# Kernel tuning notes

Measured on AMD Instinct MI355X. Metric: run time of the kernel, lower is better.

Reference implementation:

```python
import jax, jax.numpy as jnp
import numpy as np
from jax import lax

D = 256      # d_model
NH = 4       # nhead == len(multi_size)
DH = D // NH # per-head dim = 64
B, H, W = 8, 32, 32
EPS_LN = 1e-5
EPS_ATT = 1e-6


def conv2d(x, w, pad):
    # x: [B,C,H,W], w: [O,I,k,k], SAME padding via pad=k//2
    return lax.conv_general_dilated(
        x, w, window_strides=(1, 1), padding=[(pad, pad), (pad, pad)],
        dimension_numbers=("NCHW", "OIHW", "NCHW"))


def layer_norm(x, g, b):
    m = jnp.mean(x, axis=-1, keepdims=True)
    v = jnp.mean((x - m) ** 2, axis=-1, keepdims=True)
    return (x - m) * lax.rsqrt(v + EPS_LN) * g + b


def setup_inputs() -> dict:
    key = jax.random.key(0)
    ks = jax.random.split(key, 20)
    s = 0.02
    inp = {
        "x": jax.random.normal(ks[0], (B, D, H, W), jnp.float32),
        "source": jax.random.normal(ks[1], (B, D, H, W), jnp.float32),
        # q projection: conv3x3 d_model -> d_model (bias-free)
        "Wq": jax.random.normal(ks[2], (D, D, 3, 3), jnp.float32) * s,
        # MultiConv k projection: kernels 1,3,5,7, each d_model -> dim
        "Wk1": jax.random.normal(ks[3], (DH, D, 1, 1), jnp.float32) * s,
        "Wk3": jax.random.normal(ks[4], (DH, D, 3, 3), jnp.float32) * s,
        "Wk5": jax.random.normal(ks[5], (DH, D, 5, 5), jnp.float32) * s,
        "Wk7": jax.random.normal(ks[6], (DH, D, 7, 7), jnp.float32) * s,
        # MultiConv v projection
        "Wv1": jax.random.normal(ks[7], (DH, D, 1, 1), jnp.float32) * s,
        "Wv3": jax.random.normal(ks[8], (DH, D, 3, 3), jnp.float32) * s,
        "Wv5": jax.random.normal(ks[9], (DH, D, 5, 5), jnp.float32) * s,
        "Wv7": jax.random.normal(ks[10], (DH, D, 7, 7), jnp.float32) * s,
        # merge linear (bias=False), stored [in,out]
        "Wm": jax.random.normal(ks[11], (D, D), jnp.float32) * s,
        "ln1_g": jnp.ones((D,), jnp.float32),
        "ln1_b": jnp.zeros((D,), jnp.float32),
        "ln2_g": jnp.ones((D,), jnp.float32),
        "ln2_b": jnp.zeros((D,), jnp.float32),
        # FF mlp: Linear(2D->2D, no bias), ReLU, Linear(2D->D, no bias); [in,out]
        "W1": jax.random.normal(ks[12], (2 * D, 2 * D), jnp.float32) * s,
        "W2": jax.random.normal(ks[13], (2 * D, D), jnp.float32) * s,
    }
    return inp


def _forward(x, source, Wq, Wk1, Wk3, Wk5, Wk7, Wv1, Wv3, Wv5, Wv7,
             Wm, ln1_g, ln1_b, ln2_g, ln2_b, W1, W2):
    b, c, h, w = x.shape
    h1, w1 = source.shape[2], source.shape[3]
    L = h * w
    S = h1 * w1

    # projections (multi-scale convs -> heads along channel)
    q = conv2d(x, Wq, 1)                                        # [b,D,h,w]
    k = jnp.concatenate([conv2d(source, Wk1, 0), conv2d(source, Wk3, 1),
                         conv2d(source, Wk5, 2), conv2d(source, Wk7, 3)], axis=1)
    v = jnp.concatenate([conv2d(source, Wv1, 0), conv2d(source, Wv3, 1),
                         conv2d(source, Wv5, 2), conv2d(source, Wv7, 3)], axis=1)

    # b c h w -> b (h w) (nhead dim) -> b L nhead dim
    q = q.transpose(0, 2, 3, 1).reshape(b, L, NH, DH)
    k = k.transpose(0, 2, 3, 1).reshape(b, S, NH, DH)
    v = v.transpose(0, 2, 3, 1).reshape(b, S, NH, DH)

    # FullAttention_vis: softmax attention map [b, L, S, nhead]
    temp = DH ** -0.5
    qk = jnp.einsum("blhd,bshd->blsh", q, k)
    attn_vis = jax.nn.softmax(qk * temp, axis=2)

    # LinearAttention (elu+1 kernel feature map)
    Qf = jax.nn.elu(q) + 1.0
    Kf = jax.nn.elu(k) + 1.0
    v_len = jnp.float32(S)
    vals = v / v_len
    KV = jnp.einsum("bshd,bshv->bhdv", Kf, vals)                # [b,NH,DH,DH]
    Z = 1.0 / (jnp.einsum("blhd,bhd->blh", Qf, Kf.sum(axis=1)) + EPS_ATT)
    msg = jnp.einsum("blhd,bhdv,blh->blhv", Qf, KV, Z) * v_len  # [b,L,NH,DH]

    # merge + norm1
    msg = layer_norm(msg.reshape(b, L, D) @ Wm, ln1_g, ln1_b)

    # FF (mlp): cat -> Linear -> ReLU -> Linear -> norm2
    xf = x.transpose(0, 2, 3, 1).reshape(b, L, c)
    ff = jax.nn.relu(jnp.concatenate([xf, msg], axis=2) @ W1) @ W2
    msg = layer_norm(ff, ln2_g, ln2_b)                          # [b,L,D]
    msg = msg.reshape(b, h, w, c).transpose(0, 3, 1, 2)         # b c h w

    out = x + msg
    # b (h0 w0) (h1 w1) c -> b c h0 w0 h1 w1
    vis = attn_vis.reshape(b, h, w, h1, w1, NH).transpose(0, 5, 1, 2, 3, 4)
    return out, vis


def reference(x, source, Wq, Wk1, Wk3, Wk5, Wk7, Wv1, Wv3, Wv5, Wv7,
              Wm, ln1_g, ln1_b, ln2_g, ln2_b, W1, W2):
    return _forward(x, source, Wq, Wk1, Wk3, Wk5, Wk7, Wv1, Wv3, Wv5, Wv7,
                    Wm, ln1_g, ln1_b, ln2_g, ln2_b, W1, W2)
```

## Files before the change

kernel.cpp:

```cpp
#include <hip/hip_runtime.h>

#define DEV __device__ __forceinline__

typedef unsigned short u16;
typedef unsigned int u32;
typedef __bf16 bf16x8 __attribute__((ext_vector_type(8)));
typedef float f32x4 __attribute__((ext_vector_type(4)));

DEV float elu1(float x) { return x > 0.f ? x + 1.f : __expf(x); }

DEV u16 f2bf(float f) {
    union { float f; unsigned u; } v; v.f = f;
    unsigned r = v.u + 0x7fffu + ((v.u >> 16) & 1u);
    return (u16)(r >> 16);
}

__global__ __launch_bounds__(256) void repack_kernel(
    const float* __restrict__ Wq,
    const float* __restrict__ Wk1, const float* __restrict__ Wk3,
    const float* __restrict__ Wk5, const float* __restrict__ Wk7,
    const float* __restrict__ Wv1, const float* __restrict__ Wv3,
    const float* __restrict__ Wv5, const float* __restrict__ Wv7,
    u16* __restrict__ wpack)
{
    int gid = blockIdx.x * 256 + threadIdx.x;
    int frag = gid >> 6, l = gid & 63;
    const float* W; int K, ocbase = 0, rel;
    if (frag < 1152) {
        W = Wq; K = 3; int slot = frag / 288; rel = frag % 288; ocbase = slot * 64;
    } else {
        int f = frag - 1152; int side = f / 2688; f %= 2688;
        if (f < 32)        { W = side ? Wv1 : Wk1; K = 1; rel = f; }
        else if (f < 320)  { W = side ? Wv3 : Wk3; K = 3; rel = f - 32; }
        else if (f < 1120) { W = side ? Wv5 : Wk5; K = 5; rel = f - 320; }
        else               { W = side ? Wv7 : Wk7; K = 7; rel = f - 1120; }
    }
    int og = rel & 3, cc = (rel >> 2) & 7, tap = rel >> 5;
    int dy = tap / K, dx = tap % K;
    int oc = ocbase + og * 16 + (l & 15);
    int c0 = cc * 32 + (l >> 4) * 8;
    u16 pk[8];
#pragma unroll
    for (int j = 0; j < 8; ++j)
        pk[j] = f2bf(W[((size_t)(oc * 256 + c0 + j) * K + dy) * K + dx]);
    *(int4*)&wpack[(size_t)frag * 512 + l * 8] = *(const int4*)pk;
}

__global__ __launch_bounds__(256) void cast_src_kernel(
    const float* __restrict__ x, const float* __restrict__ src,
    u16* __restrict__ xbh, u16* __restrict__ sbh)
{
    __shared__ float lds[32 * 129];
    const int i = blockIdx.x, t = threadIdx.x;
    const int inp = i >> 9, rem = i & 511;
    const int b = rem >> 6, cc = (rem >> 3) & 7, pxb = rem & 7;
    const float* in = (inp ? src : x) + ((size_t)b * 256 + cc * 32) * 1024 + pxb * 128;
    u16* outp = (inp ? sbh : xbh) + (size_t)b * 262144 + (size_t)cc * 32768 + pxb * 128 * 32;
#pragma unroll
    for (int u = 0; u < 4; ++u) {
        int unit = t + u * 256;
        int r = unit >> 5, px4 = unit & 31;
        float4 v = *(const float4*)(in + (size_t)r * 1024 + px4 * 4);
        lds[r * 129 + px4 * 4 + 0] = v.x;
        lds[r * 129 + px4 * 4 + 1] = v.y;
        lds[r * 129 + px4 * 4 + 2] = v.z;
        lds[r * 129 + px4 * 4 + 3] = v.w;
    }
    __syncthreads();
#pragma unroll
    for (int u = 0; u < 2; ++u) {
        int unit = t + u * 256;
        int px = unit >> 2, cg = unit & 3;
        u16 pk[8];
#pragma unroll
        for (int j = 0; j < 8; ++j) pk[j] = f2bf(lds[(cg * 8 + j) * 129 + px]);
        *(int4*)&outp[px * 32 + cg * 8] = *(const int4*)pk;
    }
}

__global__ __launch_bounds__(256) void cast_qk_kernel(
    const float* __restrict__ qb, const float* __restrict__ kb,
    u16* __restrict__ qbt, u16* __restrict__ kbt)
{
    __shared__ float lds[64 * 65];
    const int i = blockIdx.x, t = threadIdx.x;
    const int inp = i >> 9, rem = i & 511;
    const int b = rem >> 6, h = (rem >> 4) & 3, pxb = rem & 15;
    const float* in = (inp ? kb : qb) + ((size_t)b * 256 + h * 64) * 1024 + pxb * 64;
    u16* outp = (inp ? kbt : qbt) + (((size_t)(b * 4 + h)) * 1024 + pxb * 64) * 64;
#pragma unroll
    for (int u = 0; u < 4; ++u) {
        int unit = t + u * 256;
        int r = unit >> 4, px4 = unit & 15;
        float4 v = *(const float4*)(in + (size_t)r * 1024 + px4 * 4);
        lds[r * 65 + px4 * 4 + 0] = v.x;
        lds[r * 65 + px4 * 4 + 1] = v.y;
        lds[r * 65 + px4 * 4 + 2] = v.z;
        lds[r * 65 + px4 * 4 + 3] = v.w;
    }
    __syncthreads();
#pragma unroll
    for (int u = 0; u < 2; ++u) {
        int unit = t + u * 256;
        int px = unit >> 3, cg = unit & 7;
        u16 pk[8];
#pragma unroll
        for (int j = 0; j < 8; ++j) pk[j] = f2bf(lds[(cg * 8 + j) * 65 + px]);
        *(int4*)&outp[px * 64 + cg * 8] = *(const int4*)pk;
    }
}

__global__ __launch_bounds__(256) void repack_ff_kernel(
    const float* __restrict__ W1, const float* __restrict__ W2,
    const float* __restrict__ Wm,
    u16* __restrict__ w1p, u16* __restrict__ w2p, u16* __restrict__ wmp)
{
    int gid = blockIdx.x * 256 + threadIdx.x;
    int f = gid >> 6, l = gid & 63;
    if (f >= 896) return;
    u16 pk[8];
    if (f < 512) {
        int ks = f >> 5, nf = f & 31;
#pragma unroll
        for (int j = 0; j < 8; ++j)
            pk[j] = f2bf(W1[(size_t)(ks * 32 + (l >> 4) * 8 + j) * 512 + nf * 16 + (l & 15)]);
        *(int4*)&w1p[(size_t)f * 512 + l * 8] = *(const int4*)pk;
    } else if (f < 768) {
        int f2 = f - 512;
        int ks = f2 >> 4, nf = f2 & 15;
#pragma unroll
        for (int j = 0; j < 8; ++j)
            pk[j] = f2bf(W2[(size_t)(ks * 32 + (l >> 4) * 8 + j) * 256 + nf * 16 + (l & 15)]);
        *(int4*)&w2p[(size_t)f2 * 512 + l * 8] = *(const int4*)pk;
    } else {
        int f3 = f - 768;
        int ks = f3 >> 4, nf = f3 & 15;
#pragma unroll
        for (int j = 0; j < 8; ++j)
            pk[j] = f2bf(Wm[(size_t)(ks * 32 + (l >> 4) * 8 + j) * 256 + nf * 16 + (l & 15)]);
        *(int4*)&wmp[(size_t)f3 * 512 + l * 8] = *(const int4*)pk;
    }
}

template<int K>
DEV void conv_mfma_body(const u16* __restrict__ srcb,
                        const u16* __restrict__ wsec,
                        float* __restrict__ dst,
                        u16* Bt, int y0, int cch0, int ncc, int t)
{
    constexpr int P = K / 2;
    const int w = t >> 6, l = t & 63;
    const int chi = l >> 4, ln = l & 15;
    const int rowbase = chi * 22 + w * 2 + 3 - P;
    const int colbase = ln + 3 - P;
    f32x4 acc[4][4];
#pragma unroll
    for (int m = 0; m < 4; ++m)
#pragma unroll
        for (int n = 0; n < 4; ++n) acc[m][n] = (f32x4){0.f, 0.f, 0.f, 0.f};

    for (int cc = 0; cc < ncc; ++cc) {
        const int ccg = cch0 + cc;
        __syncthreads();
#pragma unroll
        for (int u = 0; u < 7; ++u) {
            int unit = t + (u << 9);
            if (unit < 2816) {
                int xv = unit & 31, r = unit >> 5;
                int yy = r % 22, ch = r / 22;
                int ygl = y0 - 3 + yy;
                int4 pk;
                if ((unsigned)ygl < 32u)
                    pk = *(const int4*)&srcb[(size_t)ccg * 32768 + (ygl * 32 + xv) * 32 + ch * 8];
                else
                    pk = (int4){0, 0, 0, 0};
                *(int4*)&Bt[((ch * 22 + yy) * 40 + xv + 3) * 8] = pk;
            } else if (unit < 3520) {
                int hu = unit - 2816;
                int hx = hu & 7; int xi = hx < 3 ? hx : hx + 32;
                int r = hu >> 3; int yy = r % 22, ch = r / 22;
                int4 z = {0, 0, 0, 0};
                *(int4*)&Bt[((ch * 22 + yy) * 40 + xi) * 8] = z;
            }
        }
        __syncthreads();
#pragma unroll
        for (int dy = 0; dy < K; ++dy) {
#pragma unroll
            for (int dx = 0; dx < K; ++dx) {
                const int tap = dy * K + dx;
                const u16* wp = wsec + ((size_t)(tap * 8 + ccg) * 4) * 512 + l * 8;
                bf16x8 a0 = *(const bf16x8*)(wp);
                bf16x8 a1 = *(const bf16x8*)(wp + 512);
                bf16x8 a2 = *(const bf16x8*)(wp + 1024);
                bf16x8 a3 = *(const bf16x8*)(wp + 1536);
                bf16x8 bf[4];
#pragma unroll
                for (int n = 0; n < 4; ++n) {
                    int row = rowbase + dy + (n >> 1);
                    int col = colbase + dx + (n & 1) * 16;
                    bf[n] = *(const bf16x8*)&Bt[(row * 40 + col) * 8];
                }
#pragma unroll
                for (int n = 0; n < 4; ++n) {
                    acc[0][n] = __builtin_amdgcn_mfma_f32_16x16x32_bf16(a0, bf[n], acc[0][n], 0, 0, 0);
                    acc[1][n] = __builtin_amdgcn_mfma_f32_16x16x32_bf16(a1, bf[n], acc[1][n], 0, 0, 0);
                    acc[2][n] = __builtin_amdgcn_mfma_f32_16x16x32_bf16(a2, bf[n], acc[2][n], 0, 0, 0);
                    acc[3][n] = __builtin_amdgcn_mfma_f32_16x16x32_bf16(a3, bf[n], acc[3][n], 0, 0, 0);
                }
            }
        }
    }
#pragma unroll
    for (int m = 0; m < 4; ++m)
#pragma unroll
        for (int n = 0; n < 4; ++n) {
            int y = y0 + w * 2 + (n >> 1);
            int px = y * 32 + (n & 1) * 16 + ln;
            int ocb = m * 16 + chi * 4;
#pragma unroll
            for (int r = 0; r < 4; ++r)
                dst[(size_t)(ocb + r) * 1024 + px] = acc[m][n][r];
        }
}

__global__ __launch_bounds__(512) void conv_mfma_kernel(
    const u16* __restrict__ xbh, const u16* __restrict__ sbh,
    const u16* __restrict__ wpack,
    float* __restrict__ qb, float* __restrict__ kb, float* __restrict__ vb,
    float* __restrict__ p5, float* __restrict__ p7)
{
    __shared__ u16 Bt[4 * 22 * 40 * 8];
    const int bx = blockIdx.x, t = threadIdx.x;
    const int g = bx & 31, b = (bx >> 5) & 7, m = bx >> 8;
    if (g < 4) {
        conv_mfma_body<3>(xbh + (size_t)b * 262144,
                          wpack + (size_t)(g * 288) * 512,
                          qb + ((size_t)b * 256 + g * 64) * 1024,
                          Bt, m * 16, 0, 8, t);
        return;
    }
    const int gs = g - 4;
    const int side = gs / 14, gg = gs % 14;
    const u16* sp = sbh + (size_t)b * 262144;
    float* fin = side ? vb : kb;
    const size_t wkb = 1152 + (size_t)side * 2688;
    if (gg == 0) {
        conv_mfma_body<1>(sp, wpack + (wkb + 0) * 512,
                          fin + ((size_t)b * 256) * 1024, Bt, m * 16, 0, 8, t);
    } else if (gg == 1) {
        conv_mfma_body<3>(sp, wpack + (wkb + 32) * 512,
                          fin + ((size_t)b * 256 + 64) * 1024, Bt, m * 16, 0, 8, t);
    } else if (gg < 6) {
        int cpart = gg - 2;
        conv_mfma_body<5>(sp, wpack + (wkb + 320) * 512,
                          p5 + (((size_t)side * 4 + cpart) * 8 + b) * 65536,
                          Bt, m * 16, cpart * 2, 2, t);
    } else {
        int cpart = gg - 6;
        conv_mfma_body<7>(sp, wpack + (wkb + 1120) * 512,
                          p7 + (((size_t)side * 8 + cpart) * 8 + b) * 65536,
                          Bt, m * 16, cpart, 1, t);
    }
}

__global__ __launch_bounds__(256) void reduce_kernel(
    const float* __restrict__ p5, const float* __restrict__ p7,
    float* __restrict__ kb, float* __restrict__ vb)
{
    int gid = blockIdx.x * 256 + threadIdx.x;
    int px4 = gid & 255;
    int rr = gid >> 8;
    int oc = rr & 63, b = (rr >> 6) & 7, head = (rr >> 9) & 1, side = rr >> 10;
    float* outb = side ? vb : kb;
    float4 s = make_float4(0.f, 0.f, 0.f, 0.f);
    if (head == 0) {
#pragma unroll
        for (int p = 0; p < 4; ++p) {
            float4 u = *((const float4*)(p5 + (((size_t)side * 4 + p) * 8 + b) * 65536 + (size_t)oc * 1024) + px4);
            s.x += u.x; s.y += u.y; s.z += u.z; s.w += u.w;
        }
        *((float4*)(outb + ((size_t)b * 256 + 128 + oc) * 1024) + px4) = s;
    } else {
#pragma unroll
        for (int p = 0; p < 8; ++p) {
            float4 u = *((const float4*)(p7 + (((size_t)side * 8 + p) * 8 + b) * 65536 + (size_t)oc * 1024) + px4);
            s.x += u.x; s.y += u.y; s.z += u.z; s.w += u.w;
        }
        *((float4*)(outb + ((size_t)b * 256 + 192 + oc) * 1024) + px4) = s;
    }
}

__global__ __launch_bounds__(512) void qk_sm_kernel(const u16* __restrict__ qbt,
                                                    const u16* __restrict__ kbt,
                                                    float* __restrict__ vis)
{
    __shared__ u16 kf[32 * 512];
    __shared__ u16 qf[4 * 512];
    __shared__ float redM[32 * 8];
    __shared__ float redS[32 * 8];
    const int t = threadIdx.x;
    const int bx = blockIdx.x;
    const int b = bx >> 7, h = (bx >> 5) & 3, l0 = (bx & 31) * 32;
    const u16* qtp = qbt + ((size_t)(b * 4 + h)) * 1024 * 64;
    const u16* ktp = kbt + ((size_t)(b * 4 + h)) * 1024 * 64;

    if (t < 256) {
        int r = t & 31, dblk = t >> 5;
        int4 pk = *(const int4*)&qtp[(size_t)(l0 + r) * 64 + dblk * 8];
        *(int4*)&qf[(((r >> 4) * 2 + (dblk >> 2)) * 64 + (dblk & 3) * 16 + (r & 15)) * 8] = pk;
    }
    __syncthreads();

    const int w = t >> 6, l = t & 63, ln = l & 15, lg = l >> 4;
    bf16x8 a[2][2];
#pragma unroll
    for (int fr = 0; fr < 2; ++fr)
#pragma unroll
        for (int ks = 0; ks < 2; ++ks)
            a[fr][ks] = *(const bf16x8*)&qf[((fr * 2 + ks) * 64 + l) * 8];

    f32x4 acc[2][4][2];
#pragma unroll
    for (int fr = 0; fr < 2; ++fr)
#pragma unroll
        for (int cc = 0; cc < 4; ++cc)
#pragma unroll
            for (int f = 0; f < 2; ++f) acc[fr][cc][f] = (f32x4){0.f, 0.f, 0.f, 0.f};

#pragma unroll
    for (int cc = 0; cc < 4; ++cc) {
        __syncthreads();
#pragma unroll
        for (int it = 0; it < 4; ++it) {
            int unit = it * 512 + t;
            int sl = unit & 255, dblk = unit >> 8;
            int4 pk = *(const int4*)&ktp[(size_t)(cc * 256 + sl) * 64 + dblk * 8];
            *(int4*)&kf[(((sl >> 4) * 2 + (dblk >> 2)) * 64 + (dblk & 3) * 16 + (sl & 15)) * 8] = pk;
        }
        __syncthreads();
#pragma unroll
        for (int f = 0; f < 2; ++f) {
            int fg = (w * 2 + f) * 2;
            bf16x8 b0 = *(const bf16x8*)&kf[((fg + 0) * 64 + l) * 8];
            bf16x8 b1 = *(const bf16x8*)&kf[((fg + 1) * 64 + l) * 8];
#pragma unroll
            for (int fr = 0; fr < 2; ++fr) {
                acc[fr][cc][f] = __builtin_amdgcn_mfma_f32_16x16x32_bf16(a[fr][0], b0, acc[fr][cc][f], 0, 0, 0);
                acc[fr][cc][f] = __builtin_amdgcn_mfma_f32_16x16x32_bf16(a[fr][1], b1, acc[fr][cc][f], 0, 0, 0);
            }
        }
    }

#pragma unroll
    for (int fr = 0; fr < 2; ++fr)
#pragma unroll
        for (int cc = 0; cc < 4; ++cc)
#pragma unroll
            for (int f = 0; f < 2; ++f)
#pragma unroll
                for (int e = 0; e < 4; ++e) acc[fr][cc][f][e] *= 0.125f;

    float rmax[2][4];
#pragma unroll
    for (int fr = 0; fr < 2; ++fr)
#pragma unroll
        for (int reg = 0; reg < 4; ++reg) {
            float m = -1e30f;
#pragma unroll
            for (int cc = 0; cc < 4; ++cc)
#pragma unroll
                for (int f = 0; f < 2; ++f) m = fmaxf(m, acc[fr][cc][f][reg]);
#pragma unroll
            for (int off = 1; off < 16; off <<= 1) m = fmaxf(m, __shfl_xor(m, off));
            if (ln == 0) redM[(fr * 16 + lg * 4 + reg) * 8 + w] = m;
            rmax[fr][reg] = m;
        }
    __syncthreads();
#pragma unroll
    for (int fr = 0; fr < 2; ++fr)
#pragma unroll
        for (int reg = 0; reg < 4; ++reg) {
            int r = fr * 16 + lg * 4 + reg;
            float m = redM[r * 8];
#pragma unroll
            for (int ww = 1; ww < 8; ++ww) m = fmaxf(m, redM[r * 8 + ww]);
            rmax[fr][reg] = m;
        }
#pragma unroll
    for (int fr = 0; fr < 2; ++fr)
#pragma unroll
        for (int reg = 0; reg < 4; ++reg) {
            float s = 0.f;
            float m = rmax[fr][reg];
#pragma unroll
            for (int cc = 0; cc < 4; ++cc)
#pragma unroll
                for (int f = 0; f < 2; ++f) {
                    float e = __expf(acc[fr][cc][f][reg] - m);
                    acc[fr][cc][f][reg] = e;
                    s += e;
                }
#pragma unroll
            for (int off = 1; off < 16; off <<= 1) s += __shfl_xor(s, off);
            if (ln == 0) redS[(fr * 16 + lg * 4 + reg) * 8 + w] = s;
        }
    __syncthreads();
    float* visp = vis + (((size_t)(b * 4 + h)) << 20);
#pragma unroll
    for (int fr = 0; fr < 2; ++fr)
#pragma unroll
        for (int reg = 0; reg < 4; ++reg) {
            int r = fr * 16 + lg * 4 + reg;
            float s = redS[r * 8] + redS[r * 8 + 1] + redS[r * 8 + 2] + redS[r * 8 + 3]
                    + redS[r * 8 + 4] + redS[r * 8 + 5] + redS[r * 8 + 6] + redS[r * 8 + 7];
            float inv = 1.f / s;
            float* vr = visp + (size_t)(l0 + r) * 1024 + w * 32 + ln;
#pragma unroll
            for (int cc = 0; cc < 4; ++cc)
#pragma unroll
                for (int f = 0; f < 2; ++f)
                    vr[cc * 256 + f * 16] = acc[fr][cc][f][reg] * inv;
        }
}

__global__ __launch_bounds__(256) void kv_kernel(const float* __restrict__ k,
                                                 const float* __restrict__ v,
                                                 float* __restrict__ KVp,
                                                 float* __restrict__ Ksump)
{
    __shared__ float4 Kt4[64*17];
    __shared__ float4 Vt4[64*16];
    float* Kt = (float*)Kt4;
    float* Vt = (float*)Vt4;
    const int t = threadIdx.x;
    const int bx = blockIdx.x;
    const int b = bx >> 4, h = (bx >> 2) & 3, ch = bx & 3;
    const float* kb = k + ((size_t)b*256 + h*64)*1024 + ch*256;
    const float* vb = v + ((size_t)b*256 + h*64)*1024 + ch*256;
    const int d = t >> 2, v0 = (t & 3) * 16;
    float4 acc[4];
#pragma unroll
    for (int j = 0; j < 4; ++j) acc[j] = make_float4(0.f, 0.f, 0.f, 0.f);
    float ks = 0.f;
    for (int st = 0; st < 4; ++st) {
        __syncthreads();
        {
            int dd = t >> 2, r0 = (t & 3) * 16;
#pragma unroll
            for (int mm = 0; mm < 4; ++mm) {
                float4 kv = *(const float4*)(kb + dd*1024 + st*64 + r0 + mm*4);
                Kt[(r0+mm*4+0)*68 + dd] = elu1(kv.x);
                Kt[(r0+mm*4+1)*68 + dd] = elu1(kv.y);
                Kt[(r0+mm*4+2)*68 + dd] = elu1(kv.z);
                Kt[(r0+mm*4+3)*68 + dd] = elu1(kv.w);
                float4 vv = *(const float4*)(vb + dd*1024 + st*64 + r0 + mm*4);
                Vt[(r0+mm*4+0)*64 + dd] = vv.x;
                Vt[(r0+mm*4+1)*64 + dd] = vv.y;
                Vt[(r0+mm*4+2)*64 + dd] = vv.z;
                Vt[(r0+mm*4+3)*64 + dd] = vv.w;
            }
        }
        __syncthreads();
#pragma unroll 8
        for (int s = 0; s < 64; ++s) {
            float kf = Kt[s*68 + d];
            const float4* vp = (const float4*)(Vt + s*64 + v0);
#pragma unroll
            for (int j = 0; j < 4; ++j) {
                float4 vv = vp[j];
                acc[j].x += kf*vv.x; acc[j].y += kf*vv.y;
                acc[j].z += kf*vv.z; acc[j].w += kf*vv.w;
            }
        }
        if (t < 64) {
#pragma unroll 8
            for (int s = 0; s < 64; ++s) ks += Kt[s*68 + t];
        }
    }
    float* op = KVp + ((size_t)((ch*32 + b*4 + h)*64 + d))*64 + v0;
#pragma unroll
    for (int j = 0; j < 4; ++j) ((float4*)op)[j] = acc[j];
    if (t < 64) Ksump[(size_t)(ch*32 + b*4 + h)*64 + t] = ks;
}

__global__ __launch_bounds__(256) void msg_kernel(const float* __restrict__ q,
                                                  const float* __restrict__ KVp,
                                                  const float* __restrict__ Ksump,
                                                  float* __restrict__ msg)
{
    __shared__ float4 kvl4[4*1028];
    __shared__ float ksl[4*65];
    float* kvl = (float*)kvl4;
    const int t = threadIdx.x;
    const int bx = blockIdx.x;
    const int b = bx >> 4;
    const int l0 = (bx & 15) * 64;
    for (int m = 0; m < 64; ++m) {
        int idx = t + 256*m;
        int hh = idx >> 12, dd = (idx >> 6) & 63, vv = idx & 63;
        float s = 0.f;
#pragma unroll
        for (int ch = 0; ch < 4; ++ch)
            s += KVp[(size_t)((ch*32 + b*4))*4096 + idx];
        kvl[hh*4112 + dd*64 + vv] = s;
    }
    {
        float s = 0.f;
#pragma unroll
        for (int ch = 0; ch < 4; ++ch)
            s += Ksump[(size_t)(ch*32 + b*4)*64 + t];
        ksl[(t >> 6)*65 + (t & 63)] = s;
    }
    __syncthreads();
    const int h = t & 3, l = l0 + (t >> 2);
    const float* qb = q + ((size_t)b*256 + h*64)*1024 + l;
    float qf[64];
#pragma unroll
    for (int dd = 0; dd < 64; ++dd) qf[dd] = elu1(qb[dd*1024]);
    float zd = 1e-6f;
#pragma unroll
    for (int dd = 0; dd < 64; ++dd) zd += qf[dd] * ksl[h*65 + dd];
    const float Z = 1.f / zd;
    float* op = msg + ((size_t)(b*1024 + l))*256 + h*64;
    for (int c0 = 0; c0 < 64; c0 += 16) {
        float4 a[4];
#pragma unroll
        for (int j = 0; j < 4; ++j) a[j] = make_float4(0.f, 0.f, 0.f, 0.f);
#pragma unroll
        for (int dd = 0; dd < 64; ++dd) {
            float qv = qf[dd];
            const float4* kp = (const float4*)(kvl + h*4112 + dd*64 + c0);
#pragma unroll
            for (int j = 0; j < 4; ++j) {
                float4 kk = kp[j];
                a[j].x += qv*kk.x; a[j].y += qv*kk.y;
                a[j].z += qv*kk.z; a[j].w += qv*kk.w;
            }
        }
#pragma unroll
        for (int j = 0; j < 4; ++j) {
            a[j].x *= Z; a[j].y *= Z; a[j].z *= Z; a[j].w *= Z;
            ((float4*)(op + c0))[j] = a[j];
        }
    }
}

__global__ __launch_bounds__(256) void merge_mfma_kernel(
    const float* __restrict__ msg, const u16* __restrict__ wmp,
    const float* __restrict__ g1, const float* __restrict__ b1,
    float* __restrict__ msgm)
{
    __shared__ u16 tile[32 * 520];
    __shared__ float redS[32 * 4];
    __shared__ float redQ[32 * 4];
    const int t = threadIdx.x;
    const int base = blockIdx.x * 32;
    const int w = t >> 6, l = t & 63, ln = l & 15, lg = l >> 4;

    {
        int r = t >> 3, cb = (t & 7) * 32;
#pragma unroll
        for (int i = 0; i < 8; ++i) {
            float4 v = *(const float4*)&msg[((size_t)(base + r)) * 256 + cb + i * 4];
            u32 p0 = (u32)f2bf(v.x) | ((u32)f2bf(v.y) << 16);
            u32 p1 = (u32)f2bf(v.z) | ((u32)f2bf(v.w) << 16);
            *(u32*)&tile[r * 520 + cb + i * 4] = p0;
            *(u32*)&tile[r * 520 + cb + i * 4 + 2] = p1;
        }
    }
    __syncthreads();

    f32x4 acc2[2][4];
#pragma unroll
    for (int fr = 0; fr < 2; ++fr)
#pragma unroll
        for (int fc = 0; fc < 4; ++fc) acc2[fr][fc] = (f32x4){0.f, 0.f, 0.f, 0.f};
    for (int ks = 0; ks < 8; ++ks) {
        bf16x8 a0 = *(const bf16x8*)&tile[(ln) * 520 + ks * 32 + lg * 8];
        bf16x8 a1 = *(const bf16x8*)&tile[(16 + ln) * 520 + ks * 32 + lg * 8];
#pragma unroll
        for (int fc = 0; fc < 4; ++fc) {
            bf16x8 bb = *(const bf16x8*)&wmp[((size_t)(ks * 16 + w * 4 + fc) * 64 + l) * 8];
            acc2[0][fc] = __builtin_amdgcn_mfma_f32_16x16x32_bf16(a0, bb, acc2[0][fc], 0, 0, 0);
            acc2[1][fc] = __builtin_amdgcn_mfma_f32_16x16x32_bf16(a1, bb, acc2[1][fc], 0, 0, 0);
        }
    }
#pragma unroll
    for (int fr = 0; fr < 2; ++fr)
#pragma unroll
        for (int reg = 0; reg < 4; ++reg) {
            float s = 0.f, qsum = 0.f;
#pragma unroll
            for (int fc = 0; fc < 4; ++fc) {
                float v = acc2[fr][fc][reg];
                s += v; qsum += v * v;
            }
#pragma unroll
            for (int off = 1; off < 16; off <<= 1) {
                s += __shfl_xor(s, off);
                qsum += __shfl_xor(qsum, off);
            }
            if (ln == 0) {
                int r = fr * 16 + lg * 4 + reg;
                redS[r * 4 + w] = s;
                redQ[r * 4 + w] = qsum;
            }
        }
    __syncthreads();
#pragma unroll
    for (int fc = 0; fc < 4; ++fc) {
        int c = w * 64 + fc * 16 + ln;
        float gg = g1[c], bb = b1[c];
#pragma unroll
        for (int fr = 0; fr < 2; ++fr)
#pragma unroll
            for (int reg = 0; reg < 4; ++reg) {
                int r = fr * 16 + lg * 4 + reg;
                float s = redS[r * 4] + redS[r * 4 + 1] + redS[r * 4 + 2] + redS[r * 4 + 3];
                float qs = redQ[r * 4] + redQ[r * 4 + 1] + redQ[r * 4 + 2] + redQ[r * 4 + 3];
                float mean = s * (1.f / 256.f);
                float rstd = rsqrtf(qs * (1.f / 256.f) - mean * mean + 1e-5f);
                msgm[((size_t)(base + r)) * 256 + c] =
                    (acc2[fr][fc][reg] - mean) * rstd * gg + bb;
            }
    }
}

__global__ __launch_bounds__(256) void ff_mfma_kernel(
    const float* __restrict__ x, const float* __restrict__ msgm,
    const u16* __restrict__ w1p, const u16* __restrict__ w2p,
    const float* __restrict__ g2, const float* __restrict__ b2,
    float* __restrict__ out)
{
    __shared__ u16 tile[32 * 520];
    __shared__ float redS[32 * 4];
    __shared__ float redQ[32 * 4];
    float* tf = (float*)tile;
    const int t = threadIdx.x;
    const int base = blockIdx.x * 32;
    const int b = base >> 10, l0 = base & 1023;
    const int w = t >> 6, l = t & 63, ln = l & 15, lg = l >> 4;

    {
        int rr = t & 31, cg = t >> 5;
        for (int cci = 0; cci < 32; ++cci) {
            int c = cci * 8 + cg;
            float v = x[((size_t)b * 256 + c) * 1024 + l0 + rr];
            tile[rr * 520 + c] = f2bf(v);
        }
        int r = t >> 3, cb = (t & 7) * 32;
#pragma unroll
        for (int i = 0; i < 8; ++i) {
            float4 v = *(const float4*)&msgm[((size_t)(base + r)) * 256 + cb + i * 4];
            u32 p0 = (u32)f2bf(v.x) | ((u32)f2bf(v.y) << 16);
            u32 p1 = (u32)f2bf(v.z) | ((u32)f2bf(v.w) << 16);
            *(u32*)&tile[r * 520 + 256 + cb + i * 4] = p0;
            *(u32*)&tile[r * 520 + 256 + cb + i * 4 + 2] = p1;
        }
    }
    __syncthreads();

    f32x4 acc[2][8];
#pragma unroll
    for (int fr = 0; fr < 2; ++fr)
#pragma unroll
        for (int fc = 0; fc < 8; ++fc) acc[fr][fc] = (f32x4){0.f, 0.f, 0.f, 0.f};
    for (int ks = 0; ks < 16; ++ks) {
        bf16x8 a0 = *(const bf16x8*)&tile[(ln) * 520 + ks * 32 + lg * 8];
        bf16x8 a1 = *(const bf16x8*)&tile[(16 + ln) * 520 + ks * 32 + lg * 8];
#pragma unroll
        for (int fc = 0; fc < 8; ++fc) {
            bf16x8 bb = *(const bf16x8*)&w1p[((size_t)(ks * 32 + w * 8 + fc) * 64 + l) * 8];
            acc[0][fc] = __builtin_amdgcn_mfma_f32_16x16x32_bf16(a0, bb, acc[0][fc], 0, 0, 0);
            acc[1][fc] = __builtin_amdgcn_mfma_f32_16x16x32_bf16(a1, bb, acc[1][fc], 0, 0, 0);
        }
    }
    __syncthreads();
#pragma unroll
    for (int fr = 0; fr < 2; ++fr)
#pragma unroll
        for (int fc = 0; fc < 8; ++fc)
#pragma unroll
            for (int reg = 0; reg < 4; ++reg) {
                int r = fr * 16 + lg * 4 + reg;
                int c = w * 128 + fc * 16 + ln;
                tile[r * 520 + c] = f2bf(fmaxf(acc[fr][fc][reg], 0.f));
            }
    __syncthreads();

    f32x4 acc2[2][4];
#pragma unroll
    for (int fr = 0; fr < 2; ++fr)
#pragma unroll
        for (int fc = 0; fc < 4; ++fc) acc2[fr][fc] = (f32x4){0.f, 0.f, 0.f, 0.f};
    for (int ks = 0; ks < 16; ++ks) {
        bf16x8 a0 = *(const bf16x8*)&tile[(ln) * 520 + ks * 32 + lg * 8];
        bf16x8 a1 = *(const bf16x8*)&tile[(16 + ln) * 520 + ks * 32 + lg * 8];
#pragma unroll
        for (int fc = 0; fc < 4; ++fc) {
            bf16x8 bb = *(const bf16x8*)&w2p[((size_t)(ks * 16 + w * 4 + fc) * 64 + l) * 8];
            acc2[0][fc] = __builtin_amdgcn_mfma_f32_16x16x32_bf16(a0, bb, acc2[0][fc], 0, 0, 0);
            acc2[1][fc] = __builtin_amdgcn_mfma_f32_16x16x32_bf16(a1, bb, acc2[1][fc], 0, 0, 0);
        }
    }
#pragma unroll
    for (int fr = 0; fr < 2; ++fr)
#pragma unroll
        for (int reg = 0; reg < 4; ++reg) {
            float s = 0.f, qsum = 0.f;
#pragma unroll
            for (int fc = 0; fc < 4; ++fc) {
                float v = acc2[fr][fc][reg];
                s += v; qsum += v * v;
            }
#pragma unroll
            for (int off = 1; off < 16; off <<= 1) {
                s += __shfl_xor(s, off);
                qsum += __shfl_xor(qsum, off);
            }
            if (ln == 0) {
                int r = fr * 16 + lg * 4 + reg;
                redS[r * 4 + w] = s;
                redQ[r * 4 + w] = qsum;
            }
        }
    __syncthreads();
    float mean[2][4], rstd[2][4];
#pragma unroll
    for (int fr = 0; fr < 2; ++fr)
#pragma unroll
        for (int reg = 0; reg < 4; ++reg) {
            int r = fr * 16 + lg * 4 + reg;
            float s = redS[r * 4] + redS[r * 4 + 1] + redS[r * 4 + 2] + redS[r * 4 + 3];
            float qs = redQ[r * 4] + redQ[r * 4 + 1] + redQ[r * 4 + 2] + redQ[r * 4 + 3];
            float m = s * (1.f / 256.f);
            mean[fr][reg] = m;
            rstd[fr][reg] = rsqrtf(qs * (1.f / 256.f) - m * m + 1e-5f);
        }
#pragma unroll
    for (int fc = 0; fc < 4; ++fc) {
        int c = w * 64 + fc * 16 + ln;
        float gg = g2[c], bb = b2[c];
#pragma unroll
        for (int fr = 0; fr < 2; ++fr)
#pragma unroll
            for (int reg = 0; reg < 4; ++reg) {
                int r = fr * 16 + lg * 4 + reg;
                tf[r * 260 + c] = (acc2[fr][fc][reg] - mean[fr][reg]) * rstd[fr][reg] * gg + bb;
            }
    }
    __syncthreads();
    {
        const float* xp = x + ((size_t)b * 256 + t) * 1024 + l0;
        float* op = out + ((size_t)b * 256 + t) * 1024 + l0;
#pragma unroll
        for (int i = 0; i < 8; ++i) {
            float4 xv = *(const float4*)(xp + i * 4);
            float4 o;
            o.x = xv.x + tf[(i * 4 + 0) * 260 + t];
            o.y = xv.y + tf[(i * 4 + 1) * 260 + t];
            o.z = xv.z + tf[(i * 4 + 2) * 260 + t];
            o.w = xv.w + tf[(i * 4 + 3) * 260 + t];
            *(float4*)(op + i * 4) = o;
        }
    }
}

extern "C" void kernel_launch(void* const* d_in, const int* in_sizes, int n_in,
                              void* d_out, int out_size, void* d_ws, size_t ws_size,
                              hipStream_t stream)
{
    const float* x    = (const float*)d_in[0];
    const float* src  = (const float*)d_in[1];
    const float* Wq   = (const float*)d_in[2];
    const float* Wk1  = (const float*)d_in[3];
    const float* Wk3  = (const float*)d_in[4];
    const float* Wk5  = (const float*)d_in[5];
    const float* Wk7  = (const float*)d_in[6];
    const float* Wv1  = (const float*)d_in[7];
    const float* Wv3  = (const float*)d_in[8];
    const float* Wv5  = (const float*)d_in[9];
    const float* Wv7  = (const float*)d_in[10];
    const float* Wm   = (const float*)d_in[11];
    const float* g1   = (const float*)d_in[12];
    const float* b1   = (const float*)d_in[13];
    const float* g2   = (const float*)d_in[14];
    const float* b2   = (const float*)d_in[15];
    const float* W1   = (const float*)d_in[16];
    const float* W2   = (const float*)d_in[17];

    float* out = (float*)d_out;
    float* vis = out + 2097152;

    float* p5 = vis;
    float* p7 = vis + 4194304;

    float* ws    = (float*)d_ws;
    float* qb    = ws;
    float* kb    = ws + 2097152;
    float* vb    = ws + 4194304;
    u16*   wpack = (u16*)(ws + 6291456);
    u16*   w1p   = (u16*)(ws + 6291456);
    u16*   w2p   = (u16*)(ws + 6422528);
    u16*   wmp   = (u16*)(ws + 6488064);
    u16*   qbt   = (u16*)(ws + 6520832);
    u16*   kbt   = (u16*)(ws + 7569408);
    u16*   xbh   = (u16*)(ws + 7962624);
    u16*   sbh   = (u16*)(ws + 9011200);
    float* msg   = ws + 7962624;
    float* msgm  = ws + 10059776;
    float* KVp   = ws + 12156928;
    float* Ksump = ws + 12681216;

    repack_kernel   <<<1632, 256, 0, stream>>>(Wq, Wk1, Wk3, Wk5, Wk7,
                                               Wv1, Wv3, Wv5, Wv7, wpack);
    cast_src_kernel <<<1024, 256, 0, stream>>>(x, src, xbh, sbh);
    conv_mfma_kernel<<<512,  512, 0, stream>>>(xbh, sbh, wpack, qb, kb, vb, p5, p7);
    reduce_kernel   <<<2048, 256, 0, stream>>>(p5, p7, kb, vb);
    repack_ff_kernel<<<224,  256, 0, stream>>>(W1, W2, Wm, w1p, w2p, wmp);
    cast_qk_kernel  <<<1024, 256, 0, stream>>>(qb, kb, qbt, kbt);
    qk_sm_kernel    <<<1024, 512, 0, stream>>>(qbt, kbt, vis);
    kv_kernel       <<<128,  256, 0, stream>>>(kb, vb, KVp, Ksump);
    msg_kernel      <<<128,  256, 0, stream>>>(qb, KVp, Ksump, msg);
    merge_mfma_kernel<<<256, 256, 0, stream>>>(msg, wmp, g1, b1, msgm);
    ff_mfma_kernel  <<<256,  256, 0, stream>>>(x, msgm, w1p, w2p, g2, b2, out);
}
```

Baseline: 291.7 us.

## Fuse merge and FF kernels, stage softmax output through LDS for coalesced stores

```diff
diff --git a/kernel.cpp b/kernel.cpp
--- a/kernel.cpp
+++ b/kernel.cpp
@@ -295,10 +295,11 @@
                                                     const u16* __restrict__ kbt,
                                                     float* __restrict__ vis)
 {
-    __shared__ u16 kf[32 * 512];
-    __shared__ u16 qf[4 * 512];
+    __shared__ u16 shbuf[36 * 512];
     __shared__ float redM[32 * 8];
     __shared__ float redS[32 * 8];
+    u16* kf = shbuf;
+    u16* qf = shbuf + 32 * 512;
     const int t = threadIdx.x;
     const int bx = blockIdx.x;
     const int b = bx >> 7, h = (bx >> 5) & 3, l0 = (bx & 31) * 32;
@@ -406,7 +407,7 @@
             if (ln == 0) redS[(fr * 16 + lg * 4 + reg) * 8 + w] = s;
         }
     __syncthreads();
-    float* visp = vis + (((size_t)(b * 4 + h)) << 20);
+    float invv[2][4];
 #pragma unroll
     for (int fr = 0; fr < 2; ++fr)
 #pragma unroll
@@ -414,14 +415,31 @@
             int r = fr * 16 + lg * 4 + reg;
             float s = redS[r * 8] + redS[r * 8 + 1] + redS[r * 8 + 2] + redS[r * 8 + 3]
                     + redS[r * 8 + 4] + redS[r * 8 + 5] + redS[r * 8 + 6] + redS[r * 8 + 7];
-            float inv = 1.f / s;
-            float* vr = visp + (size_t)(l0 + r) * 1024 + w * 32 + ln;
-#pragma unroll
-            for (int cc = 0; cc < 4; ++cc)
+            invv[fr][reg] = 1.f / s;
+        }
+    float* outT = (float*)shbuf;
+    float* visp = vis + (((size_t)(b * 4 + h)) << 20);
+#pragma unroll
+    for (int cc = 0; cc < 4; ++cc) {
+        __syncthreads();
+#pragma unroll
+        for (int fr = 0; fr < 2; ++fr)
+#pragma unroll
+            for (int reg = 0; reg < 4; ++reg) {
+                int r = fr * 16 + lg * 4 + reg;
 #pragma unroll
                 for (int f = 0; f < 2; ++f)
-                    vr[cc * 256 + f * 16] = acc[fr][cc][f][reg] * inv;
-        }
+                    outT[r * 260 + w * 32 + f * 16 + ln] = acc[fr][cc][f][reg] * invv[fr][reg];
+            }
+        __syncthreads();
+#pragma unroll
+        for (int u = 0; u < 4; ++u) {
+            int unit = u * 512 + t;
+            int r = unit >> 6, c4 = unit & 63;
+            float4 v = *(const float4*)&outT[r * 260 + c4 * 4];
+            *(float4*)&visp[(size_t)(l0 + r) * 1024 + cc * 256 + c4 * 4] = v;
+        }
+    }
 }
 
 __global__ __launch_bounds__(256) void kv_kernel(const float* __restrict__ k,
@@ -546,216 +564,169 @@
     }
 }
 
-__global__ __launch_bounds__(256) void merge_mfma_kernel(
-    const float* __restrict__ msg, const u16* __restrict__ wmp,
+__global__ __launch_bounds__(256) void ff_fused_kernel(
+    const float* __restrict__ x, const float* __restrict__ msg,
+    const u16* __restrict__ wmp,
+    const u16* __restrict__ w1p, const u16* __restrict__ w2p,
     const float* __restrict__ g1, const float* __restrict__ b1,
-    float* __restrict__ msgm)
-{
-    __shared__ u16 tile[32 * 520];
-    __shared__ float redS[32 * 4];
-    __shared__ float redQ[32 * 4];
+    const float* __restrict__ g2, const float* __restrict__ b2,
+    float* __restrict__ out)
+{
+    __shared__ u16 tile[16 * 520];
+    __shared__ u16 mtile[16 * 264];
+    __shared__ float redS[16 * 4];
+    __shared__ float redQ[16 * 4];
+    float* tf = (float*)tile;
     const int t = threadIdx.x;
-    const int base = blockIdx.x * 32;
+    const int base = blockIdx.x * 16;
+    const int b = base >> 10, l0 = base & 1023;
     const int w = t >> 6, l = t & 63, ln = l & 15, lg = l >> 4;
 
     {
-        int r = t >> 3, cb = (t & 7) * 32;
-#pragma unroll
-        for (int i = 0; i < 8; ++i) {
+        int rr = t & 15, cg = t >> 4;
+        for (int cci = 0; cci < 16; ++cci) {
+            int c = cci * 16 + cg;
+            tile[rr * 520 + c] = f2bf(x[((size_t)b * 256 + c) * 1024 + l0 + rr]);
+        }
+        int r = t >> 4, cb = (t & 15) * 16;
+#pragma unroll
+        for (int i = 0; i < 4; ++i) {
             float4 v = *(const float4*)&msg[((size_t)(base + r)) * 256 + cb + i * 4];
             u32 p0 = (u32)f2bf(v.x) | ((u32)f2bf(v.y) << 16);
             u32 p1 = (u32)f2bf(v.z) | ((u32)f2bf(v.w) << 16);
-            *(u32*)&tile[r * 520 + cb + i * 4] = p0;
-            *(u32*)&tile[r * 520 + cb + i * 4 + 2] = p1;
-        }
-    }
-    __syncthreads();
-
-    f32x4 acc2[2][4];
-#pragma unroll
-    for (int fr = 0; fr < 2; ++fr)
-#pragma unroll
-        for (int fc = 0; fc < 4; ++fc) acc2[fr][fc] = (f32x4){0.f, 0.f, 0.f, 0.f};
+            *(u32*)&mtile[r * 264 + cb + i * 4] = p0;
+            *(u32*)&mtile[r * 264 + cb + i * 4 + 2] = p1;
+        }
+    }
+    __syncthreads();
+
+    f32x4 accm[4];
+#pragma unroll
+    for (int fc = 0; fc < 4; ++fc) accm[fc] = (f32x4){0.f, 0.f, 0.f, 0.f};
     for (int ks = 0; ks < 8; ++ks) {
-        bf16x8 a0 = *(const bf16x8*)&tile[(ln) * 520 + ks * 32 + lg * 8];
-        bf16x8 a1 = *(const bf16x8*)&tile[(16 + ln) * 520 + ks * 32 + lg * 8];
+        bf16x8 a0 = *(const bf16x8*)&mtile[ln * 264 + ks * 32 + lg * 8];
 #pragma unroll
         for (int fc = 0; fc < 4; ++fc) {
             bf16x8 bb = *(const bf16x8*)&wmp[((size_t)(ks * 16 + w * 4 + fc) * 64 + l) * 8];
-            acc2[0][fc] = __builtin_amdgcn_mfma_f32_16x16x32_bf16(a0, bb, acc2[0][fc], 0, 0, 0);
-            acc2[1][fc] = __builtin_amdgcn_mfma_f32_16x16x32_bf16(a1, bb, acc2[1][fc], 0, 0, 0);
-        }
-    }
-#pragma unroll
-    for (int fr = 0; fr < 2; ++fr)
-#pragma unroll
-        for (int reg = 0; reg < 4; ++reg) {
-            float s = 0.f, qsum = 0.f;
-#pragma unroll
-            for (int fc = 0; fc < 4; ++fc) {
-                float v = acc2[fr][fc][reg];
-                s += v; qsum += v * v;
-            }
-#pragma unroll
-            for (int off = 1; off < 16; off <<= 1) {
-                s += __shfl_xor(s, off);
-                qsum += __shfl_xor(qsum, off);
-            }
-            if (ln == 0) {
-                int r = fr * 16 + lg * 4 + reg;
-                redS[r * 4 + w] = s;
-                redQ[r * 4 + w] = qsum;
-            }
-        }
+            accm[fc] = __builtin_amdgcn_mfma_f32_16x16x32_bf16(a0, bb, accm[fc], 0, 0, 0);
+        }
+    }
+#pragma unroll
+    for (int reg = 0; reg < 4; ++reg) {
+        float s = 0.f, qsum = 0.f;
+#pragma unroll
+        for (int fc = 0; fc < 4; ++fc) {
+            float v = accm[fc][reg];
+            s += v; qsum += v * v;
+        }
+#pragma unroll
+        for (int off = 1; off < 16; off <<= 1) {
+            s += __shfl_xor(s, off);
+            qsum += __shfl_xor(qsum, off);
+        }
+        if (ln == 0) {
+            int r = lg * 4 + reg;
+            redS[r * 4 + w] = s;
+            redQ[r * 4 + w] = qsum;
+        }
+    }
     __syncthreads();
 #pragma unroll
     for (int fc = 0; fc < 4; ++fc) {
         int c = w * 64 + fc * 16 + ln;
         float gg = g1[c], bb = b1[c];
 #pragma unroll
-        for (int fr = 0; fr < 2; ++fr)
-#pragma unroll
-            for (int reg = 0; reg < 4; ++reg) {
-                int r = fr * 16 + lg * 4 + reg;
-                float s = redS[r * 4] + redS[r * 4 + 1] + redS[r * 4 + 2] + redS[r * 4 + 3];
-                float qs = redQ[r * 4] + redQ[r * 4 + 1] + redQ[r * 4 + 2] + redQ[r * 4 + 3];
-                float mean = s * (1.f / 256.f);
-                float rstd = rsqrtf(qs * (1.f / 256.f) - mean * mean + 1e-5f);
-                msgm[((size_t)(base + r)) * 256 + c] =
-                    (acc2[fr][fc][reg] - mean) * rstd * gg + bb;
-            }
-    }
-}
-
-__global__ __launch_bounds__(256) void ff_mfma_kernel(
-    const float* __restrict__ x, const float* __restrict__ msgm,
-    const u16* __restrict__ w1p, const u16* __restrict__ w2p,
-    const float* __restrict__ g2, const float* __restrict__ b2,
-    float* __restrict__ out)
-{
-    __shared__ u16 tile[32 * 520];
-    __shared__ float redS[32 * 4];
-    __shared__ float redQ[32 * 4];
-    float* tf = (float*)tile;
-    const int t = threadIdx.x;
-    const int base = blockIdx.x * 32;
-    const int b = base >> 10, l0 = base & 1023;
-    const int w = t >> 6, l = t & 63, ln = l & 15, lg = l >> 4;
-
-    {
-        int rr = t & 31, cg = t >> 5;
-        for (int cci = 0; cci < 32; ++cci) {
-            int c = cci * 8 + cg;
-            float v = x[((size_t)b * 256 + c) * 1024 + l0 + rr];
-            tile[rr * 520 + c] = f2bf(v);
-        }
-        int r = t >> 3, cb = (t & 7) * 32;
-#pragma unroll
-        for (int i = 0; i < 8; ++i) {
-            float4 v = *(const float4*)&msgm[((size_t)(base + r)) * 256 + cb + i * 4];
-            u32 p0 = (u32)f2bf(v.x) | ((u32)f2bf(v.y) << 16);
-            u32 p1 = (u32)f2bf(v.z) | ((u32)f2bf(v.w) << 16);
-            *(u32*)&tile[r * 520 + 256 + cb + i * 4] = p0;
-            *(u32*)&tile[r * 520 + 256 + cb + i * 4 + 2] = p1;
-        }
-    }
-    __syncthreads();
-
-    f32x4 acc[2][8];
-#pragma unroll
-    for (int fr = 0; fr < 2; ++fr)
-#pragma unroll
-        for (int fc = 0; fc < 8; ++fc) acc[fr][fc] = (f32x4){0.f, 0.f, 0.f, 0.f};
+        for (int reg = 0; reg < 4; ++reg) {
+            int r = lg * 4 + reg;
+            float s = redS[r * 4] + redS[r * 4 + 1] + redS[r * 4 + 2] + redS[r * 4 + 3];
+            float qs = redQ[r * 4] + redQ[r * 4 + 1] + redQ[r * 4 + 2] + redQ[r * 4 + 3];
+            float mean = s * (1.f / 256.f);
+            float rstd = rsqrtf(qs * (1.f / 256.f) - mean * mean + 1e-5f);
+            tile[r * 520 + 256 + c] = f2bf((accm[fc][reg] - mean) * rstd * gg + bb);
+        }
+    }
+    __syncthreads();
+
+    f32x4 acc1[8];
+#pragma unroll
+    for (int fc = 0; fc < 8; ++fc) acc1[fc] = (f32x4){0.f, 0.f, 0.f, 0.f};
     for (int ks = 0; ks < 16; ++ks) {
-        bf16x8 a0 = *(const bf16x8*)&tile[(ln) * 520 + ks * 32 + lg * 8];
-        bf16x8 a1 = *(const bf16x8*)&tile[(16 + ln) * 520 + ks * 32 + lg * 8];
+        bf16x8 a0 = *(const bf16x8*)&tile[ln * 520 + ks * 32 + lg * 8];
 #pragma unroll
         for (int fc = 0; fc < 8; ++fc) {
             bf16x8 bb = *(const bf16x8*)&w1p[((size_t)(ks * 32 + w * 8 + fc) * 64 + l) * 8];
-            acc[0][fc] = __builtin_amdgcn_mfma_f32_16x16x32_bf16(a0, bb, acc[0][fc], 0, 0, 0);
-            acc[1][fc] = __builtin_amdgcn_mfma_f32_16x16x32_bf16(a1, bb, acc[1][fc], 0, 0, 0);
-        }
-    }
-    __syncthreads();
-#pragma unroll
-    for (int fr = 0; fr < 2; ++fr)
-#pragma unroll
-        for (int fc = 0; fc < 8; ++fc)
-#pragma unroll
-            for (int reg = 0; reg < 4; ++reg) {
-                int r = fr * 16 + lg * 4 + reg;
-                int c = w * 128 + fc * 16 + ln;
-                tile[r * 520 + c] = f2bf(fmaxf(acc[fr][fc][reg], 0.f));
-            }
-    __syncthreads();
-
-    f32x4 acc2[2][4];
-#pragma unroll
-    for (int fr = 0; fr < 2; ++fr)
-#pragma unroll
-        for (int fc = 0; fc < 4; ++fc) acc2[fr][fc] = (f32x4){0.f, 0.f, 0.f, 0.f};
+            acc1[fc] = __builtin_amdgcn_mfma_f32_16x16x32_bf16(a0, bb, acc1[fc], 0, 0, 0);
+        }
+    }
+    __syncthreads();
+#pragma unroll
+    for (int fc = 0; fc < 8; ++fc)
+#pragma unroll
+        for (int reg = 0; reg < 4; ++reg) {
+            int r = lg * 4 + reg;
+            int c = w * 128 + fc * 16 + ln;
+            tile[r * 520 + c] = f2bf(fmaxf(acc1[fc][reg], 0.f));
+        }
+    __syncthreads();
+
+    f32x4 acc2[4];
+#pragma unroll
+    for (int fc = 0; fc < 4; ++fc) acc2[fc] = (f32x4){0.f, 0.f, 0.f, 0.f};
     for (int ks = 0; ks < 16; ++ks) {
-        bf16x8 a0 = *(const bf16x8*)&tile[(ln) * 520 + ks * 32 + lg * 8];
-        bf16x8 a1 = *(const bf16x8*)&tile[(16 + ln) * 520 + ks * 32 + lg * 8];
+        bf16x8 a0 = *(const bf16x8*)&tile[ln * 520 + ks * 32 + lg * 8];
 #pragma unroll
         for (int fc = 0; fc < 4; ++fc) {
             bf16x8 bb = *(const bf16x8*)&w2p[((size_t)(ks * 16 + w * 4 + fc) * 64 + l) * 8];
-            acc2[0][fc] = __builtin_amdgcn_mfma_f32_16x16x32_bf16(a0, bb, acc2[0][fc], 0, 0, 0);
-            acc2[1][fc] = __builtin_amdgcn_mfma_f32_16x16x32_bf16(a1, bb, acc2[1][fc], 0, 0, 0);
-        }
-    }
-#pragma unroll
-    for (int fr = 0; fr < 2; ++fr)
-#pragma unroll
-        for (int reg = 0; reg < 4; ++reg) {
-            float s = 0.f, qsum = 0.f;
-#pragma unroll
-            for (int fc = 0; fc < 4; ++fc) {
-                float v = acc2[fr][fc][reg];
-                s += v; qsum += v * v;
-            }
-#pragma unroll
-            for (int off = 1; off < 16; off <<= 1) {
-                s += __shfl_xor(s, off);
-                qsum += __shfl_xor(qsum, off);
-            }
-            if (ln == 0) {
-                int r = fr * 16 + lg * 4 + reg;
-                redS[r * 4 + w] = s;
-                redQ[r * 4 + w] = qsum;
-            }
-        }
-    __syncthreads();
-    float mean[2][4], rstd[2][4];
-#pragma unroll
-    for (int fr = 0; fr < 2; ++fr)
-#pragma unroll
-        for (int reg = 0; reg < 4; ++reg) {
-            int r = fr * 16 + lg * 4 + reg;
-            float s = redS[r * 4] + redS[r * 4 + 1] + redS[r * 4 + 2] + redS[r * 4 + 3];
-            float qs = redQ[r * 4] + redQ[r * 4 + 1] + redQ[r * 4 + 2] + redQ[r * 4 + 3];
-            float m = s * (1.f / 256.f);
-            mean[fr][reg] = m;
-            rstd[fr][reg] = rsqrtf(qs * (1.f / 256.f) - m * m + 1e-5f);
-        }
+            acc2[fc] = __builtin_amdgcn_mfma_f32_16x16x32_bf16(a0, bb, acc2[fc], 0, 0, 0);
+        }
+    }
+#pragma unroll
+    for (int reg = 0; reg < 4; ++reg) {
+        float s = 0.f, qsum = 0.f;
+#pragma unroll
+        for (int fc = 0; fc < 4; ++fc) {
+            float v = acc2[fc][reg];
+            s += v; qsum += v * v;
+        }
+#pragma unroll
+        for (int off = 1; off < 16; off <<= 1) {
+            s += __shfl_xor(s, off);
+            qsum += __shfl_xor(qsum, off);
+        }
+        if (ln == 0) {
+            int r = lg * 4 + reg;
+            redS[r * 4 + w] = s;
+            redQ[r * 4 + w] = qsum;
+        }
+    }
+    __syncthreads();
+    float mean[4], rstd[4];
+#pragma unroll
+    for (int reg = 0; reg < 4; ++reg) {
+        int r = lg * 4 + reg;
+        float s = redS[r * 4] + redS[r * 4 + 1] + redS[r * 4 + 2] + redS[r * 4 + 3];
+        float qs = redQ[r * 4] + redQ[r * 4 + 1] + redQ[r * 4 + 2] + redQ[r * 4 + 3];
+        float m = s * (1.f / 256.f);
+        mean[reg] = m;
+        rstd[reg] = rsqrtf(qs * (1.f / 256.f) - m * m + 1e-5f);
+    }
+    __syncthreads();
 #pragma unroll
     for (int fc = 0; fc < 4; ++fc) {
         int c = w * 64 + fc * 16 + ln;
         float gg = g2[c], bb = b2[c];
 #pragma unroll
-        for (int fr = 0; fr < 2; ++fr)
-#pragma unroll
-            for (int reg = 0; reg < 4; ++reg) {
-                int r = fr * 16 + lg * 4 + reg;
-                tf[r * 260 + c] = (acc2[fr][fc][reg] - mean[fr][reg]) * rstd[fr][reg] * gg + bb;
-            }
+        for (int reg = 0; reg < 4; ++reg) {
+            int r = lg * 4 + reg;
+            tf[r * 260 + c] = (acc2[fc][reg] - mean[reg]) * rstd[reg] * gg + bb;
+        }
     }
     __syncthreads();
     {
         const float* xp = x + ((size_t)b * 256 + t) * 1024 + l0;
         float* op = out + ((size_t)b * 256 + t) * 1024 + l0;
 #pragma unroll
-        for (int i = 0; i < 8; ++i) {
+        for (int i = 0; i < 4; ++i) {
             float4 xv = *(const float4*)(xp + i * 4);
             float4 o;
             o.x = xv.x + tf[(i * 4 + 0) * 260 + t];
@@ -809,7 +780,6 @@
     u16*   xbh   = (u16*)(ws + 7962624);
     u16*   sbh   = (u16*)(ws + 9011200);
     float* msg   = ws + 7962624;
-    float* msgm  = ws + 10059776;
     float* KVp   = ws + 12156928;
     float* Ksump = ws + 12681216;
 
@@ -823,6 +793,6 @@
     qk_sm_kernel    <<<1024, 512, 0, stream>>>(qbt, kbt, vis);
     kv_kernel       <<<128,  256, 0, stream>>>(kb, vb, KVp, Ksump);
     msg_kernel      <<<128,  256, 0, stream>>>(qb, KVp, Ksump, msg);
-    merge_mfma_kernel<<<256, 256, 0, stream>>>(msg, wmp, g1, b1, msgm);
-    ff_mfma_kernel  <<<256,  256, 0, stream>>>(x, msgm, w1p, w2p, g2, b2, out);
-}
+    ff_fused_kernel <<<512,  256, 0, stream>>>(x, msg, wmp, w1p, w2p,
+                                               g1, b1, g2, b2, out);
+}
```

Result: faster. 274.1 us (-6.0%).
